# Kernel optimization log

Hardware: AMD Instinct MI355X
Metric: run time of the kernel (lower is better)

Reference implementation:

```python
import jax, jax.numpy as jnp
import numpy as np
import math

B, L, D = 2, 2048, 1024
H, DH, R, MAX_ORDER = 16, 64, 512, 5
NUM_BASIS = MAX_ORDER + 1  # min(basis_rank=512, 6)


def setup_inputs() -> dict:
    key = jax.random.key(0)
    ks = jax.random.split(key, 8)
    s = 0.02
    return {
        "hidden_states": jax.random.normal(ks[0], (B, L, D), jnp.float32),
        "attention_mask": jnp.zeros((B, 1, 1, L), jnp.float32),
        "Wq": jax.random.normal(ks[1], (D, D), jnp.float32) * s,
        "bq": jnp.zeros((D,), jnp.float32),
        "Wk": jax.random.normal(ks[2], (D, D), jnp.float32) * s,
        "bk": jnp.zeros((D,), jnp.float32),
        "Wv": jax.random.normal(ks[3], (D, D), jnp.float32) * s,
        "bv": jnp.zeros((D,), jnp.float32),
        "q_proj_weight": jax.random.normal(ks[4], (H, DH, R), jnp.float32) / math.sqrt(DH),
        "k_proj_weight": jax.random.normal(ks[5], (H, DH, R), jnp.float32) / math.sqrt(DH),
        "coefficients": jax.random.normal(ks[6], (H, NUM_BASIS), jnp.float32) * s,
    }


def _basis_bias(coefficients, seq_len, dtype):
    # rel[i, j] = (j - i) / (L - 1), clamped to [-1, 1]; DCT basis cos(pi * k * x)
    pos = jnp.arange(seq_len, dtype=dtype)
    x = jnp.clip((pos[None, :] - pos[:, None]) / max(seq_len - 1, 1), -1.0, 1.0)
    k = jnp.arange(NUM_BASIS, dtype=dtype)
    tk = jnp.cos(jnp.pi * x[..., None] * k)  # [L, L, K]
    return jnp.einsum('hk,ijk->hij', coefficients, tk)  # [H, L, L]


def reference(hidden_states, attention_mask, Wq, bq, Wk, bk, Wv, bv,
              q_proj_weight, k_proj_weight, coefficients):
    b, l, _ = hidden_states.shape

    def shape_heads(x):
        return x.reshape(b, l, H, DH).transpose(0, 2, 1, 3)  # [B, H, L, DH]

    q = shape_heads(hidden_states @ Wq.T + bq)
    k = shape_heads(hidden_states @ Wk.T + bk)
    v = shape_heads(hidden_states @ Wv.T + bv)

    qp = jnp.einsum('bhld,hdr->bhlr', q, q_proj_weight)
    kp = jnp.einsum('bhld,hdr->bhlr', k, k_proj_weight)
    scores = jnp.einsum('bhlr,bhmr->bhlm', qp, kp) / math.sqrt(R)

    bias = _basis_bias(coefficients, l, scores.dtype)
    scores = scores + bias[None] + attention_mask

    probs = jax.nn.softmax(scores, axis=-1)  # dropout is identity in eval
    ctx = jnp.einsum('bhlm,bhmd->bhld', probs, v)
    return ctx.transpose(0, 2, 1, 3).reshape(b, l, H * DH)
```

## Files before the change

kernel.cpp:

```cpp
#include <hip/hip_runtime.h>


typedef unsigned short ushort_t;
typedef unsigned long long ull_t;
typedef __attribute__((ext_vector_type(8))) short bf16x8;
typedef __attribute__((ext_vector_type(4))) float f32x4;

#define LOG2E 1.4426950408889634f
#define PI_F 3.14159265358979323846f

__device__ inline f32x4 mfma16(bf16x8 a, bf16x8 b, f32x4 c) {
  return __builtin_amdgcn_mfma_f32_16x16x32_bf16(a, b, c, 0, 0, 0);
}
__device__ inline void load_lds16(const void* g, void* l) {
  __builtin_amdgcn_global_load_lds((const __attribute__((address_space(1))) unsigned int*)g,
                                   (__attribute__((address_space(3))) unsigned int*)l, 16, 0, 0);
}
__device__ inline ushort_t f2bf(float f) {
  union { float f; unsigned int u; } v; v.f = f;
  unsigned int u = v.u;
  return (ushort_t)((u + 0x7fffu + ((u >> 16) & 1u)) >> 16);
}
__device__ inline unsigned cvt_pk_bf16(float lo, float hi) {
  unsigned r;
  asm("v_cvt_pk_bf16_f32 %0, %1, %2" : "=v"(r) : "v"(lo), "v"(hi));
  return r;
}
#if __has_builtin(__builtin_amdgcn_exp2f)
__device__ inline float exp2_(float x) { return __builtin_amdgcn_exp2f(x); }
#else
__device__ inline float exp2_(float x) { return exp2f(x); }
#endif

__global__ __launch_bounds__(256) void k_pre0(
    const float* __restrict__ kpw, const float* __restrict__ coef,
    const float* __restrict__ maskp,
    float* __restrict__ kpwT, ushort_t* __restrict__ ke, ushort_t* __restrict__ qe) {
  const int blk = blockIdx.x, tid = threadIdx.x;
  if (blk < 128) {
    __shared__ float tile[64][65];
    int h = blk >> 3, rt = blk & 7;
    const float* src = kpw + ((size_t)h * 64) * 512 + rt * 64;
    #pragma unroll
    for (int i = 0; i < 4; i++) {
      int idx = i * 256 + tid;
      int row = idx >> 4, c4 = idx & 15;
      float4 v = *(const float4*)(src + (size_t)row * 512 + c4 * 4);
      *(float4*)(&tile[row][c4 * 4]) = v;
    }
    __syncthreads();
    float* dst = kpwT + ((size_t)h * 512 + rt * 64) * 64;
    #pragma unroll
    for (int i = 0; i < 4; i++) {
      int idx = i * 256 + tid;
      int r = idx >> 4, c4 = idx & 15;
      float4 v = {tile[c4 * 4 + 0][r], tile[c4 * 4 + 1][r],
                  tile[c4 * 4 + 2][r], tile[c4 * 4 + 3][r]};
      *(float4*)(dst + (size_t)r * 64 + c4 * 4) = v;
    }
  } else if (blk < 144) {
    int i = (blk - 128) * 256 + tid;
    int bb = i >> 11, m = i & 2047;
    float base = PI_F * (float)m * (1.0f / 2047.0f);
    ushort_t row[32];
    row[0] = f2bf(1.0f);
    #pragma unroll
    for (int k = 1; k <= 5; k++) {
      float a = base * (float)k;
      row[2 * k - 1] = f2bf(cosf(a));
      row[2 * k]     = f2bf(sinf(a));
    }
    row[11] = f2bf(maskp[bb * 2048 + m] * LOG2E);
    #pragma unroll
    for (int j = 12; j < 32; j++) row[j] = 0;
    ull_t* dst = (ull_t*)(ke + ((size_t)(bb * 2048 + m)) * 32);
    #pragma unroll
    for (int j = 0; j < 4; j++) {
      ull_t pk = 0;
      #pragma unroll
      for (int e = 0; e < 4; e++) pk |= (ull_t)row[j * 4 + e] << (16 * e);
      dst[j] = pk;
    }
  } else {
    int i = (blk - 144) * 256 + tid;
    int h = i >> 11, q = i & 2047;
    float base = PI_F * (float)q * (1.0f / 2047.0f);
    ushort_t row[32];
    row[0] = f2bf(coef[h * 6] * LOG2E);
    #pragma unroll
    for (int k = 1; k <= 5; k++) {
      float ck = coef[h * 6 + k] * LOG2E;
      float a = base * (float)k;
      row[2 * k - 1] = f2bf(ck * cosf(a));
      row[2 * k]     = f2bf(ck * sinf(a));
    }
    row[11] = f2bf(1.0f);
    #pragma unroll
    for (int j = 12; j < 32; j++) row[j] = 0;
    ull_t* dst = (ull_t*)(qe + ((size_t)(h * 2048 + q)) * 32);
    #pragma unroll
    for (int j = 0; j < 4; j++) {
      ull_t pk = 0;
      #pragma unroll
      for (int e = 0; e < 4; e++) pk |= (ull_t)row[j * 4 + e] << (16 * e);
      dst[j] = pk;
    }
  }
}

__global__ __launch_bounds__(256) void k_prep(
    const float* __restrict__ hidden, const float* __restrict__ Wk,
    const float* __restrict__ Wv, const float* __restrict__ qpw,
    const float* __restrict__ kpwT,
    ushort_t* __restrict__ hb, ushort_t* __restrict__ w3, float* __restrict__ Ah) {
  const int blk = blockIdx.x, tid = threadIdx.x;
  if (blk < 64) {
    int h = blk >> 2, db = (blk & 3) * 16;
    int dp = tid & 63, d0 = db + (tid >> 6) * 4;
    float acc[4] = {0.f, 0.f, 0.f, 0.f};
    const float* kT = kpwT + (size_t)h * 512 * 64 + dp;
    const float* qr = qpw + ((size_t)h * 64 + d0) * 512;
    for (int r = 0; r < 512; r += 4) {
      float4 wk = {kT[(size_t)(r + 0) * 64], kT[(size_t)(r + 1) * 64],
                   kT[(size_t)(r + 2) * 64], kT[(size_t)(r + 3) * 64]};
      #pragma unroll
      for (int i = 0; i < 4; i++) {
        float4 wq = *(const float4*)(qr + i * 512 + r);
        acc[i] += wq.x * wk.x + wq.y * wk.y + wq.z * wk.z + wq.w * wk.w;
      }
    }
    #pragma unroll
    for (int i = 0; i < 4; i++)
      Ah[((size_t)h * 64 + d0 + i) * 64 + dp] = acc[i] * (0.044194173824159216f * LOG2E);
  } else {
    const float* in;
    ushort_t* out;
    int base = blk - 64;
    if (base < 4096) { in = hidden; out = hb; }
    else if (base < 5120) { in = Wk; out = w3 + 1048576; base -= 4096; }
    else { in = Wv; out = w3 + 2097152; base -= 5120; }
    int i = (base * 256 + tid) * 4;
    float4 v = *(const float4*)(in + i);
    unsigned long long pk = (unsigned long long)f2bf(v.x)
                          | ((unsigned long long)f2bf(v.y) << 16)
                          | ((unsigned long long)f2bf(v.z) << 32)
                          | ((unsigned long long)f2bf(v.w) << 48);
    *(unsigned long long*)(out + i) = pk;
  }
}

__global__ __launch_bounds__(256) void k_wq(
    const float* __restrict__ Wq, const float* __restrict__ Ah,
    const float* __restrict__ bq, ushort_t* __restrict__ w3, float* __restrict__ bq2) {
  __shared__ float wq_s[64][65];
  __shared__ float ah_s[64][65];
  int h = blockIdx.y, ct = blockIdx.x;
  int t = threadIdx.x;
  #pragma unroll
  for (int i = 0; i < 16; i++) {
    int idx = i * 256 + t, r = idx >> 6, c = idx & 63;
    wq_s[r][c] = Wq[((size_t)h * 64 + r) * 1024 + ct * 64 + c];
    ah_s[r][c] = Ah[((size_t)h * 64 + r) * 64 + c];
  }
  __syncthreads();
  int dp = t >> 2, cg = (t & 3) * 16;
  float acc[16];
  #pragma unroll
  for (int j = 0; j < 16; j++) acc[j] = 0.f;
  for (int d = 0; d < 64; d++) {
    float a = ah_s[d][dp];
    #pragma unroll
    for (int j = 0; j < 16; j++) acc[j] += a * wq_s[d][cg + j];
  }
  ushort_t* orow = w3 + ((size_t)h * 64 + dp) * 1024 + ct * 64 + cg;
  #pragma unroll
  for (int j = 0; j < 16; j += 4) {
    unsigned long long pk = (unsigned long long)f2bf(acc[j])
                          | ((unsigned long long)f2bf(acc[j + 1]) << 16)
                          | ((unsigned long long)f2bf(acc[j + 2]) << 32)
                          | ((unsigned long long)f2bf(acc[j + 3]) << 48);
    *(unsigned long long*)(orow + j) = pk;
  }
  if (ct == 0 && t < 64) {
    float bsum = 0.f;
    for (int d = 0; d < 64; d++) bsum += bq[h * 64 + d] * ah_s[d][t];
    bq2[h * 64 + t] = bsum;
  }
}

__global__ __launch_bounds__(256) void k_gemm(
    const ushort_t* __restrict__ hb, const ushort_t* __restrict__ w3,
    const float* __restrict__ bq2, const float* __restrict__ bk,
    const float* __restrict__ bv, ushort_t* __restrict__ qk, ushort_t* __restrict__ vT) {
  __shared__ ushort_t Asm[128 * 32];
  __shared__ ushort_t Bsm[128 * 32];
  const int tid = threadIdx.x, w = tid >> 6, l = tid & 63, g = l >> 4, l15 = l & 15;
  const int raw = blockIdx.x;
  const int id = (raw & 7) * 96 + (raw >> 3);
  const bool isv = id >= 512;
  int bx, by;
  const ushort_t *Aptr, *Bptr;
  if (!isv) { bx = id & 31; by = id >> 5; Aptr = hb; Bptr = w3; }
  else { int id2 = id - 512; bx = id2 & 7; by = id2 >> 3; Aptr = w3 + 2048 * 1024; Bptr = hb; }
  const int mbase = bx * 128, nbase = by * 128;
  const int wrow = (w >> 1) * 64, wcol = (w & 1) * 64;
  f32x4 zero4 = {0.f, 0.f, 0.f, 0.f};
  f32x4 acc[4][4];
  #pragma unroll
  for (int i = 0; i < 4; i++)
    #pragma unroll
    for (int j = 0; j < 4; j++) acc[i][j] = zero4;

  for (int kt = 0; kt < 32; ++kt) {
    __syncthreads();
    #pragma unroll
    for (int i = 0; i < 2; i++) {
      int inst = w * 2 + i;
      int r = inst * 16 + (l >> 2);
      int cs = (l & 3) ^ (r & 3);
      load_lds16(Aptr + (size_t)(mbase + r) * 1024 + kt * 32 + cs * 8, &Asm[inst * 512]);
      load_lds16(Bptr + (size_t)(nbase + r) * 1024 + kt * 32 + cs * 8, &Bsm[inst * 512]);
    }
    __syncthreads();
    bf16x8 a[4], bfr[4];
    #pragma unroll
    for (int rt = 0; rt < 4; rt++) {
      int r = wrow + rt * 16 + l15;
      a[rt] = *(const bf16x8*)(&Asm[r * 32 + ((g ^ (r & 3)) << 3)]);
    }
    #pragma unroll
    for (int ct = 0; ct < 4; ct++) {
      int r = wcol + ct * 16 + l15;
      bfr[ct] = *(const bf16x8*)(&Bsm[r * 32 + ((g ^ (r & 3)) << 3)]);
    }
    #pragma unroll
    for (int rt = 0; rt < 4; rt++)
      #pragma unroll
      for (int ct = 0; ct < 4; ct++)
        acc[rt][ct] = mfma16(a[rt], bfr[ct], acc[rt][ct]);
  }
  if (!isv) {
    #pragma unroll
    for (int ct = 0; ct < 4; ct++) {
      int n = nbase + wcol + ct * 16 + l15;
      float bias = (n < 1024) ? bq2[n] : bk[n - 1024];
      #pragma unroll
      for (int rt = 0; rt < 4; rt++)
        #pragma unroll
        for (int reg = 0; reg < 4; reg++) {
          int m = mbase + wrow + rt * 16 + g * 4 + reg;
          qk[(size_t)m * 2048 + n] = f2bf(acc[rt][ct][reg] + bias);
        }
    }
  } else {
    #pragma unroll
    for (int rt = 0; rt < 4; rt++)
      #pragma unroll
      for (int reg = 0; reg < 4; reg++) {
        int dg = mbase + wrow + rt * 16 + g * 4 + reg;
        float bias = bv[dg];
        ushort_t* vrow = vT + ((size_t)(dg >> 6)) * 131072 + (size_t)(dg & 63) * 2048;
        #pragma unroll
        for (int ct = 0; ct < 4; ct++) {
          int mg = nbase + wcol + ct * 16 + l15;
          vrow[((size_t)(mg >> 11)) * 2097152 + (mg & 2047)] = f2bf(acc[rt][ct][reg] + bias);
        }
      }
  }
}

__global__ __launch_bounds__(256, 4) void k_attn(
    const ushort_t* __restrict__ qk, const ushort_t* __restrict__ vT,
    const ushort_t* __restrict__ qe, const ushort_t* __restrict__ ke,
    float* __restrict__ out) {
  __shared__ ushort_t k_sm[2][64][64];
  __shared__ ushort_t vt_sm[2][64][64];
  __shared__ ushort_t ke_sm[2][64][32];
  const int tid = threadIdx.x, w = tid >> 6, l = tid & 63, g = l >> 4, l15 = l & 15;
  const int e01 = l15 & 3, a0 = (l15 >> 2) & 1;
  const int lr = l >> 3, lc = l & 7;
  const int bid = blockIdx.x, xcd = bid & 7, slot = bid >> 3;
  const int bh = xcd * 4 + (slot & 3), qb = slot >> 2;
  const int b = bh >> 4, h = bh & 15;
  const int wrow = qb * 64 + w * 16;
  const int q = wrow + l15;

  const ushort_t* kbase = qk + 1024 + h * 64;
  const ushort_t* vT_bh = vT + (size_t)bh * 64 * 2048;
  const ushort_t* ke_b = ke + (size_t)b * 2048 * 32;

  auto stage = [&](int t, int bi) {
    int kvb = t * 64;
    #pragma unroll
    for (int ii = 0; ii < 2; ii++) {
      int m = w * 16 + ii * 8 + lr;
      int sc = lc ^ ((lr & 3) | (ii << 2));
      load_lds16(kbase + (size_t)(b * 2048 + kvb + m) * 2048 + sc * 8,
                 &k_sm[bi][w * 16 + ii * 8][0]);
    }
    #pragma unroll
    for (int ii = 0; ii < 2; ii++) {
      int d = w * 16 + ii * 8 + lr;
      int sc = lc ^ ((lr & 3) | (ii << 2));
      load_lds16(vT_bh + (size_t)d * 2048 + kvb + sc * 8,
                 &vt_sm[bi][w * 16 + ii * 8][0]);
    }
    {
      int ml = l >> 2, c = l & 3;
      load_lds16(ke_b + (size_t)(kvb + w * 16 + ml) * 32 + ((c ^ (ml & 3)) << 3),
                 &ke_sm[bi][w * 16][0]);
    }
  };

  stage(0, 0);

  bf16x8 qf[2], qfe;
  {
    const ushort_t* qpr = qk + (size_t)(b * 2048 + q) * 2048 + h * 64 + g * 8;
    qf[0] = *(const bf16x8*)(qpr);
    qf[1] = *(const bf16x8*)(qpr + 32);
    qfe = *(const bf16x8*)(qe + ((size_t)(h * 2048 + q)) * 32 + g * 8);
  }

  f32x4 zero4 = {0.f, 0.f, 0.f, 0.f};
  f32x4 ctx[4];
  float lrow = 0.f;
  #pragma unroll
  for (int dt = 0; dt < 4; dt++) ctx[dt] = zero4;

  __syncthreads();

  for (int t = 0; t < 32; t++) {
    const int bi = t & 1;
    if (t < 31) stage(t + 1, bi ^ 1);

    f32x4 ST[4];
    #pragma unroll
    for (int mt = 0; mt < 4; mt++) ST[mt] = zero4;
    #pragma unroll
    for (int ks = 0; ks < 2; ks++) {
      #pragma unroll
      for (int mt = 0; mt < 4; mt++) {
        int mr = (mt >> 1) * 32 + (l15 >> 2) * 8 + (mt & 1) * 4 + e01;
        int pc = (ks * 4 + g) ^ (e01 | (a0 << 2));
        bf16x8 af = *(const bf16x8*)(&k_sm[bi][mr][pc * 8]);
        ST[mt] = mfma16(af, qf[ks], ST[mt]);
      }
    }
    #pragma unroll
    for (int mt = 0; mt < 4; mt++) {
      int mr = (mt >> 1) * 32 + (l15 >> 2) * 8 + (mt & 1) * 4 + e01;
      bf16x8 af = *(const bf16x8*)(&ke_sm[bi][mr][(g ^ e01) * 8]);
      ST[mt] = mfma16(af, qfe, ST[mt]);
    }

    float pv[4][4];
    #pragma unroll
    for (int mt = 0; mt < 4; mt++) {
      pv[mt][0] = exp2_(ST[mt][0]);
      pv[mt][1] = exp2_(ST[mt][1]);
      pv[mt][2] = exp2_(ST[mt][2]);
      pv[mt][3] = exp2_(ST[mt][3]);
      lrow += pv[mt][0] + pv[mt][1] + pv[mt][2] + pv[mt][3];
    }
    bf16x8 pf[2];
    {
      union { unsigned u[4]; bf16x8 v; } pk0, pk1;
      pk0.u[0] = cvt_pk_bf16(pv[0][0], pv[0][1]);
      pk0.u[1] = cvt_pk_bf16(pv[0][2], pv[0][3]);
      pk0.u[2] = cvt_pk_bf16(pv[1][0], pv[1][1]);
      pk0.u[3] = cvt_pk_bf16(pv[1][2], pv[1][3]);
      pk1.u[0] = cvt_pk_bf16(pv[2][0], pv[2][1]);
      pk1.u[1] = cvt_pk_bf16(pv[2][2], pv[2][3]);
      pk1.u[2] = cvt_pk_bf16(pv[3][0], pv[3][1]);
      pk1.u[3] = cvt_pk_bf16(pv[3][2], pv[3][3]);
      pf[0] = pk0.v;
      pf[1] = pk1.v;
    }

    #pragma unroll
    for (int kp = 0; kp < 2; kp++) {
      #pragma unroll
      for (int dt = 0; dt < 4; dt++) {
        int d = dt * 16 + l15;
        int pc = (kp * 4 + g) ^ (e01 | (((l15 >> 3) & 1) << 2));
        bf16x8 vf = *(const bf16x8*)(&vt_sm[bi][d][pc * 8]);
        ctx[dt] = mfma16(vf, pf[kp], ctx[dt]);
      }
    }

    __syncthreads();
  }

  lrow += __shfl_xor(lrow, 16);
  lrow += __shfl_xor(lrow, 32);
  float inv = 1.0f / lrow;
  float* op = out + ((size_t)(b * 2048 + q)) * 1024 + h * 64 + g * 4;
  #pragma unroll
  for (int dt = 0; dt < 4; dt++) {
    float4 o = {ctx[dt][0] * inv, ctx[dt][1] * inv, ctx[dt][2] * inv, ctx[dt][3] * inv};
    *(float4*)(op + dt * 16) = o;
  }
}

extern "C" void kernel_launch(void* const* d_in, const int* in_sizes, int n_in,
                              void* d_out, int out_size, void* d_ws, size_t ws_size,
                              hipStream_t stream) {
  const float* hidden = (const float*)d_in[0];
  const float* maskp  = (const float*)d_in[1];
  const float* Wq     = (const float*)d_in[2];
  const float* bq     = (const float*)d_in[3];
  const float* Wk     = (const float*)d_in[4];
  const float* bk     = (const float*)d_in[5];
  const float* Wv     = (const float*)d_in[6];
  const float* bv     = (const float*)d_in[7];
  const float* qpw    = (const float*)d_in[8];
  const float* kpw    = (const float*)d_in[9];
  const float* coef   = (const float*)d_in[10];

  char* ws = (char*)d_ws;
  ushort_t* keb   = (ushort_t*)(ws);
  ushort_t* hb    = (ushort_t*)(ws + 262144);
  ushort_t* w3    = (ushort_t*)(ws + 8650752);
  float*    Ah    = (float*)(ws + 14942208);
  float*    bq2   = (float*)(ws + 15204352);
  ushort_t* qeb   = (ushort_t*)(ws + 15208448);
  ushort_t* qkb   = (ushort_t*)(ws + 17305600);
  ushort_t* vTb   = (ushort_t*)(ws + 34082816);
  float*    kpwT  = (float*)(ws + 42471424);

  k_pre0<<<272, 256, 0, stream>>>(kpw, coef, maskp, kpwT, keb, qeb);
  k_prep<<<6208, 256, 0, stream>>>(hidden, Wk, Wv, qpw, kpwT, hb, w3, Ah);
  k_wq<<<dim3(16, 16), 256, 0, stream>>>(Wq, Ah, bq, w3, bq2);
  k_gemm<<<768, 256, 0, stream>>>(hb, w3, bq2, bk, bv, qkb, vTb);
  k_attn<<<1024, 256, 0, stream>>>(qkb, vTb, qeb, keb, (float*)d_out);
}
```

Before: 146.6 us.

## Merge pre0 into prep, load bias key rows into registers, raise attn occupancy

Removes the k_pre0 launch. Its kpw transpose is replaced by staging kpw tiles through LDS inside the Ah computation, and its DCT/mask table generation moves into extra blocks of k_prep. In the attention kernel the small per-key bias rows (ke) are now prefetched straight from global memory into registers one tile ahead instead of being staged through LDS. This frees LDS, and the launch-bounds occupancy hint goes from 4 to 5. The changes save one launch and some LDS traffic, at the cost of more registers per thread and possible spills under the tighter occupancy bound.

```diff
diff --git a/kernel.cpp b/kernel.cpp
--- a/kernel.cpp
+++ b/kernel.cpp
@@ -32,107 +32,45 @@
 __device__ inline float exp2_(float x) { return exp2f(x); }
 #endif
 
-__global__ __launch_bounds__(256) void k_pre0(
-    const float* __restrict__ kpw, const float* __restrict__ coef,
-    const float* __restrict__ maskp,
-    float* __restrict__ kpwT, ushort_t* __restrict__ ke, ushort_t* __restrict__ qe) {
-  const int blk = blockIdx.x, tid = threadIdx.x;
-  if (blk < 128) {
-    __shared__ float tile[64][65];
-    int h = blk >> 3, rt = blk & 7;
-    const float* src = kpw + ((size_t)h * 64) * 512 + rt * 64;
-    #pragma unroll
-    for (int i = 0; i < 4; i++) {
-      int idx = i * 256 + tid;
-      int row = idx >> 4, c4 = idx & 15;
-      float4 v = *(const float4*)(src + (size_t)row * 512 + c4 * 4);
-      *(float4*)(&tile[row][c4 * 4]) = v;
-    }
-    __syncthreads();
-    float* dst = kpwT + ((size_t)h * 512 + rt * 64) * 64;
-    #pragma unroll
-    for (int i = 0; i < 4; i++) {
-      int idx = i * 256 + tid;
-      int r = idx >> 4, c4 = idx & 15;
-      float4 v = {tile[c4 * 4 + 0][r], tile[c4 * 4 + 1][r],
-                  tile[c4 * 4 + 2][r], tile[c4 * 4 + 3][r]};
-      *(float4*)(dst + (size_t)r * 64 + c4 * 4) = v;
-    }
-  } else if (blk < 144) {
-    int i = (blk - 128) * 256 + tid;
-    int bb = i >> 11, m = i & 2047;
-    float base = PI_F * (float)m * (1.0f / 2047.0f);
-    ushort_t row[32];
-    row[0] = f2bf(1.0f);
-    #pragma unroll
-    for (int k = 1; k <= 5; k++) {
-      float a = base * (float)k;
-      row[2 * k - 1] = f2bf(cosf(a));
-      row[2 * k]     = f2bf(sinf(a));
-    }
-    row[11] = f2bf(maskp[bb * 2048 + m] * LOG2E);
-    #pragma unroll
-    for (int j = 12; j < 32; j++) row[j] = 0;
-    ull_t* dst = (ull_t*)(ke + ((size_t)(bb * 2048 + m)) * 32);
-    #pragma unroll
-    for (int j = 0; j < 4; j++) {
-      ull_t pk = 0;
-      #pragma unroll
-      for (int e = 0; e < 4; e++) pk |= (ull_t)row[j * 4 + e] << (16 * e);
-      dst[j] = pk;
-    }
-  } else {
-    int i = (blk - 144) * 256 + tid;
-    int h = i >> 11, q = i & 2047;
-    float base = PI_F * (float)q * (1.0f / 2047.0f);
-    ushort_t row[32];
-    row[0] = f2bf(coef[h * 6] * LOG2E);
-    #pragma unroll
-    for (int k = 1; k <= 5; k++) {
-      float ck = coef[h * 6 + k] * LOG2E;
-      float a = base * (float)k;
-      row[2 * k - 1] = f2bf(ck * cosf(a));
-      row[2 * k]     = f2bf(ck * sinf(a));
-    }
-    row[11] = f2bf(1.0f);
-    #pragma unroll
-    for (int j = 12; j < 32; j++) row[j] = 0;
-    ull_t* dst = (ull_t*)(qe + ((size_t)(h * 2048 + q)) * 32);
-    #pragma unroll
-    for (int j = 0; j < 4; j++) {
-      ull_t pk = 0;
-      #pragma unroll
-      for (int e = 0; e < 4; e++) pk |= (ull_t)row[j * 4 + e] << (16 * e);
-      dst[j] = pk;
-    }
-  }
-}
-
 __global__ __launch_bounds__(256) void k_prep(
     const float* __restrict__ hidden, const float* __restrict__ Wk,
     const float* __restrict__ Wv, const float* __restrict__ qpw,
-    const float* __restrict__ kpwT,
-    ushort_t* __restrict__ hb, ushort_t* __restrict__ w3, float* __restrict__ Ah) {
+    const float* __restrict__ kpw, const float* __restrict__ coef,
+    const float* __restrict__ maskp,
+    ushort_t* __restrict__ hb, ushort_t* __restrict__ w3, float* __restrict__ Ah,
+    ushort_t* __restrict__ ke, ushort_t* __restrict__ qe) {
+  __shared__ float tile[64][65];
   const int blk = blockIdx.x, tid = threadIdx.x;
   if (blk < 64) {
     int h = blk >> 2, db = (blk & 3) * 16;
     int dp = tid & 63, d0 = db + (tid >> 6) * 4;
     float acc[4] = {0.f, 0.f, 0.f, 0.f};
-    const float* kT = kpwT + (size_t)h * 512 * 64 + dp;
+    const float* kh = kpw + (size_t)h * 64 * 512;
     const float* qr = qpw + ((size_t)h * 64 + d0) * 512;
-    for (int r = 0; r < 512; r += 4) {
-      float4 wk = {kT[(size_t)(r + 0) * 64], kT[(size_t)(r + 1) * 64],
-                   kT[(size_t)(r + 2) * 64], kT[(size_t)(r + 3) * 64]};
+    for (int rc = 0; rc < 8; rc++) {
+      __syncthreads();
       #pragma unroll
       for (int i = 0; i < 4; i++) {
-        float4 wq = *(const float4*)(qr + i * 512 + r);
-        acc[i] += wq.x * wk.x + wq.y * wk.y + wq.z * wk.z + wq.w * wk.w;
+        int idx = i * 256 + tid;
+        int d = idx >> 4, c4 = idx & 15;
+        float4 v = *(const float4*)(kh + (size_t)d * 512 + rc * 64 + c4 * 4);
+        *(float4*)(&tile[d][c4 * 4]) = v;
+      }
+      __syncthreads();
+      for (int rr = 0; rr < 64; rr += 4) {
+        float4 wk = *(const float4*)(&tile[dp][rr]);
+        int r = rc * 64 + rr;
+        #pragma unroll
+        for (int i = 0; i < 4; i++) {
+          float4 wq = *(const float4*)(qr + i * 512 + r);
+          acc[i] += wq.x * wk.x + wq.y * wk.y + wq.z * wk.z + wq.w * wk.w;
+        }
       }
     }
     #pragma unroll
     for (int i = 0; i < 4; i++)
       Ah[((size_t)h * 64 + d0 + i) * 64 + dp] = acc[i] * (0.044194173824159216f * LOG2E);
-  } else {
+  } else if (blk < 6208) {
     const float* in;
     ushort_t* out;
     int base = blk - 64;
@@ -141,11 +79,56 @@
     else { in = Wv; out = w3 + 2097152; base -= 5120; }
     int i = (base * 256 + tid) * 4;
     float4 v = *(const float4*)(in + i);
-    unsigned long long pk = (unsigned long long)f2bf(v.x)
-                          | ((unsigned long long)f2bf(v.y) << 16)
-                          | ((unsigned long long)f2bf(v.z) << 32)
-                          | ((unsigned long long)f2bf(v.w) << 48);
-    *(unsigned long long*)(out + i) = pk;
+    ull_t pk = (ull_t)f2bf(v.x) | ((ull_t)f2bf(v.y) << 16)
+             | ((ull_t)f2bf(v.z) << 32) | ((ull_t)f2bf(v.w) << 48);
+    *(ull_t*)(out + i) = pk;
+  } else if (blk < 6224) {
+    int i = (blk - 6208) * 256 + tid;
+    int bb = i >> 11, m = i & 2047;
+    float base = PI_F * (float)m * (1.0f / 2047.0f);
+    ushort_t row[32];
+    row[0] = f2bf(1.0f);
+    #pragma unroll
+    for (int k = 1; k <= 5; k++) {
+      float a = base * (float)k;
+      row[2 * k - 1] = f2bf(cosf(a));
+      row[2 * k]     = f2bf(sinf(a));
+    }
+    row[11] = f2bf(maskp[bb * 2048 + m] * LOG2E);
+    #pragma unroll
+    for (int j = 12; j < 32; j++) row[j] = 0;
+    ull_t* dst = (ull_t*)(ke + ((size_t)(bb * 2048 + m)) * 32);
+    #pragma unroll
+    for (int j = 0; j < 4; j++) {
+      ull_t pk = 0;
+      #pragma unroll
+      for (int e = 0; e < 4; e++) pk |= (ull_t)row[j * 4 + e] << (16 * e);
+      dst[j] = pk;
+    }
+  } else {
+    int i = (blk - 6224) * 256 + tid;
+    int h = i >> 11, q = i & 2047;
+    float base = PI_F * (float)q * (1.0f / 2047.0f);
+    ushort_t row[32];
+    row[0] = f2bf(coef[h * 6] * LOG2E);
+    #pragma unroll
+    for (int k = 1; k <= 5; k++) {
+      float ck = coef[h * 6 + k] * LOG2E;
+      float a = base * (float)k;
+      row[2 * k - 1] = f2bf(ck * cosf(a));
+      row[2 * k]     = f2bf(ck * sinf(a));
+    }
+    row[11] = f2bf(1.0f);
+    #pragma unroll
+    for (int j = 12; j < 32; j++) row[j] = 0;
+    ull_t* dst = (ull_t*)(qe + ((size_t)(h * 2048 + q)) * 32);
+    #pragma unroll
+    for (int j = 0; j < 4; j++) {
+      ull_t pk = 0;
+      #pragma unroll
+      for (int e = 0; e < 4; e++) pk |= (ull_t)row[j * 4 + e] << (16 * e);
+      dst[j] = pk;
+    }
   }
 }
 
@@ -175,11 +158,9 @@
   ushort_t* orow = w3 + ((size_t)h * 64 + dp) * 1024 + ct * 64 + cg;
   #pragma unroll
   for (int j = 0; j < 16; j += 4) {
-    unsigned long long pk = (unsigned long long)f2bf(acc[j])
-                          | ((unsigned long long)f2bf(acc[j + 1]) << 16)
-                          | ((unsigned long long)f2bf(acc[j + 2]) << 32)
-                          | ((unsigned long long)f2bf(acc[j + 3]) << 48);
-    *(unsigned long long*)(orow + j) = pk;
+    ull_t pk = (ull_t)f2bf(acc[j]) | ((ull_t)f2bf(acc[j + 1]) << 16)
+             | ((ull_t)f2bf(acc[j + 2]) << 32) | ((ull_t)f2bf(acc[j + 3]) << 48);
+    *(ull_t*)(orow + j) = pk;
   }
   if (ct == 0 && t < 64) {
     float bsum = 0.f;
@@ -269,13 +250,12 @@
   }
 }
 
-__global__ __launch_bounds__(256, 4) void k_attn(
+__global__ __launch_bounds__(256, 5) void k_attn(
     const ushort_t* __restrict__ qk, const ushort_t* __restrict__ vT,
     const ushort_t* __restrict__ qe, const ushort_t* __restrict__ ke,
     float* __restrict__ out) {
   __shared__ ushort_t k_sm[2][64][64];
   __shared__ ushort_t vt_sm[2][64][64];
-  __shared__ ushort_t ke_sm[2][64][32];
   const int tid = threadIdx.x, w = tid >> 6, l = tid & 63, g = l >> 4, l15 = l & 15;
   const int e01 = l15 & 3, a0 = (l15 >> 2) & 1;
   const int lr = l >> 3, lc = l & 7;
@@ -289,6 +269,11 @@
   const ushort_t* vT_bh = vT + (size_t)bh * 64 * 2048;
   const ushort_t* ke_b = ke + (size_t)b * 2048 * 32;
 
+  const int mr0 = (l15 >> 2) * 8 + e01;
+  const int mr1 = mr0 + 4;
+  const int mr2 = mr0 + 32;
+  const int mr3 = mr0 + 36;
+
   auto stage = [&](int t, int bi) {
     int kvb = t * 64;
     #pragma unroll
@@ -304,11 +289,6 @@
       int sc = lc ^ ((lr & 3) | (ii << 2));
       load_lds16(vT_bh + (size_t)d * 2048 + kvb + sc * 8,
                  &vt_sm[bi][w * 16 + ii * 8][0]);
-    }
-    {
-      int ml = l >> 2, c = l & 3;
-      load_lds16(ke_b + (size_t)(kvb + w * 16 + ml) * 32 + ((c ^ (ml & 3)) << 3),
-                 &ke_sm[bi][w * 16][0]);
     }
   };
 
@@ -321,6 +301,10 @@
     qf[1] = *(const bf16x8*)(qpr + 32);
     qfe = *(const bf16x8*)(qe + ((size_t)(h * 2048 + q)) * 32 + g * 8);
   }
+  bf16x8 kef0 = *(const bf16x8*)(ke_b + (size_t)mr0 * 32 + g * 8);
+  bf16x8 kef1 = *(const bf16x8*)(ke_b + (size_t)mr1 * 32 + g * 8);
+  bf16x8 kef2 = *(const bf16x8*)(ke_b + (size_t)mr2 * 32 + g * 8);
+  bf16x8 kef3 = *(const bf16x8*)(ke_b + (size_t)mr3 * 32 + g * 8);
 
   f32x4 zero4 = {0.f, 0.f, 0.f, 0.f};
   f32x4 ctx[4];
@@ -332,7 +316,15 @@
 
   for (int t = 0; t < 32; t++) {
     const int bi = t & 1;
-    if (t < 31) stage(t + 1, bi ^ 1);
+    bf16x8 kn0, kn1, kn2, kn3;
+    if (t < 31) {
+      stage(t + 1, bi ^ 1);
+      const ushort_t* kp = ke_b + (size_t)(t + 1) * 64 * 32 + g * 8;
+      kn0 = *(const bf16x8*)(kp + (size_t)mr0 * 32);
+      kn1 = *(const bf16x8*)(kp + (size_t)mr1 * 32);
+      kn2 = *(const bf16x8*)(kp + (size_t)mr2 * 32);
+      kn3 = *(const bf16x8*)(kp + (size_t)mr3 * 32);
+    }
 
     f32x4 ST[4];
     #pragma unroll
@@ -347,12 +339,10 @@
         ST[mt] = mfma16(af, qf[ks], ST[mt]);
       }
     }
-    #pragma unroll
-    for (int mt = 0; mt < 4; mt++) {
-      int mr = (mt >> 1) * 32 + (l15 >> 2) * 8 + (mt & 1) * 4 + e01;
-      bf16x8 af = *(const bf16x8*)(&ke_sm[bi][mr][(g ^ e01) * 8]);
-      ST[mt] = mfma16(af, qfe, ST[mt]);
-    }
+    ST[0] = mfma16(kef0, qfe, ST[0]);
+    ST[1] = mfma16(kef1, qfe, ST[1]);
+    ST[2] = mfma16(kef2, qfe, ST[2]);
+    ST[3] = mfma16(kef3, qfe, ST[3]);
 
     float pv[4][4];
     #pragma unroll
@@ -389,6 +379,7 @@
       }
     }
 
+    kef0 = kn0; kef1 = kn1; kef2 = kn2; kef3 = kn3;
     __syncthreads();
   }
 
@@ -427,10 +418,9 @@
   ushort_t* qeb   = (ushort_t*)(ws + 15208448);
   ushort_t* qkb   = (ushort_t*)(ws + 17305600);
   ushort_t* vTb   = (ushort_t*)(ws + 34082816);
-  float*    kpwT  = (float*)(ws + 42471424);
-
-  k_pre0<<<272, 256, 0, stream>>>(kpw, coef, maskp, kpwT, keb, qeb);
-  k_prep<<<6208, 256, 0, stream>>>(hidden, Wk, Wv, qpw, kpwT, hb, w3, Ah);
+
+  k_prep<<<6352, 256, 0, stream>>>(hidden, Wk, Wv, qpw, kpw, coef, maskp,
+                                   hb, w3, Ah, keb, qeb);
   k_wq<<<dim3(16, 16), 256, 0, stream>>>(Wq, Ah, bq, w3, bq2);
   k_gemm<<<768, 256, 0, stream>>>(hb, w3, bq2, bk, bv, qkb, vTb);
   k_attn<<<1024, 256, 0, stream>>>(qkb, vTb, qeb, keb, (float*)d_out);
```

Result: slower. 149.8 us (+2.2%).
